# Optimization experiments

Hardware: AMD Instinct MI355X
Metric: run time of the kernel (lower is better)

## Reference

```python
import jax, jax.numpy as jnp
import numpy as np

B, T, D, H = 16, 1024, 512, 8
DH = D // H
NEG = jnp.float32(-2**32 + 1)


def setup_inputs() -> dict:
    key = jax.random.key(0)
    ks = jax.random.split(key, 9)
    s = 1.0 / np.sqrt(D)
    return {
        "queries": jax.random.normal(ks[0], (B, T, D), jnp.float32),
        "keys": jax.random.normal(ks[1], (B, T, D), jnp.float32),
        "value": jax.random.normal(ks[2], (B, T, D), jnp.float32),
        "Wq": jax.random.normal(ks[3], (D, D), jnp.float32) * s,
        "bq": jnp.zeros((D,), jnp.float32),
        "Wk": jax.random.normal(ks[4], (D, D), jnp.float32) * s,
        "bk": jnp.zeros((D,), jnp.float32),
        "Wv": jax.random.normal(ks[5], (D, D), jnp.float32) * s,
        "bv": jnp.zeros((D,), jnp.float32),
    }


def reference(queries, keys, value, Wq, bq, Wk, bk, Wv, bv):
    b, tq, d = queries.shape
    tk = keys.shape[1]
    # linear projections
    Q = queries @ Wq + bq   # [B,Tq,D]
    K = keys @ Wk + bk      # [B,Tk,D]
    V = value @ Wv + bv     # [B,Tk,D]
    # split heads: chunk along feature dim == reshape to [B,T,H,DH]
    Qh = Q.reshape(b, tq, H, DH)
    Kh = K.reshape(b, tk, H, DH)
    Vh = V.reshape(b, tk, H, DH)
    scores = jnp.einsum("bqhd,bkhd->bhqk", Qh, Kh) / jnp.sqrt(jnp.float32(DH))
    # key padding mask: rows of keys summing to 0 are padding
    key_mask = jnp.sign(jnp.abs(keys.sum(axis=-1)))      # [B,Tk]
    scores = jnp.where(key_mask[:, None, None, :] == 0, NEG, scores)
    # causal mask
    causal = jnp.tril(jnp.ones((tq, tk), jnp.float32))   # [Tq,Tk]
    scores = jnp.where(causal[None, None, :, :] == 0, NEG, scores)
    probs = jax.nn.softmax(scores, axis=-1)              # [B,H,Tq,Tk]
    # query padding mask (applied AFTER softmax, as in source)
    query_mask = jnp.sign(jnp.abs(queries.sum(axis=-1)))  # [B,Tq]
    probs = probs * query_mask[:, None, :, None]
    # dropout_rate=0.0 -> identity
    out = jnp.einsum("bhqk,bkhd->bqhd", probs, Vh).reshape(b, tq, d)
    return out + queries  # residual
```

## Files before the change

### kernel.cpp

```cpp
#include <hip/hip_runtime.h>
#include <hip/hip_bf16.h>

#define B_ 16
#define T_ 1024
#define D_ 512
#define H_ 8
#define M_ (B_ * T_)

typedef __attribute__((ext_vector_type(4))) float f32x4;
typedef __attribute__((ext_vector_type(8))) short bf16x8;
typedef __attribute__((ext_vector_type(4))) short bf16x4;

__device__ __forceinline__ void gld_lds16(const void* g, void* l) {
    __builtin_amdgcn_global_load_lds((const __attribute__((address_space(1))) void*)g,
                                     (__attribute__((address_space(3))) void*)l, 16, 0, 0);
}

__device__ __forceinline__ short f2bf(float f) {
    union { float f; unsigned u; } v; v.f = f;
    unsigned r = v.u + 0x7FFF + ((v.u >> 16) & 1);
    return (short)(r >> 16);
}

__global__ void prep_kernel(const float* __restrict__ q, const float* __restrict__ k,
                            const float* __restrict__ v,
                            const float* __restrict__ Wq, const float* __restrict__ Wk,
                            const float* __restrict__ Wv,
                            short* __restrict__ Xbf, short* __restrict__ WtAll,
                            float* __restrict__ qm, float* __restrict__ kb) {
    __shared__ float tile[64][65];
    const int t = threadIdx.x;
    const int mat = blockIdx.y;
    if (blockIdx.x < 64) {
        const float* W = (mat == 0) ? Wq : (mat == 1) ? Wk : Wv;
        short* Wt = WtAll + (size_t)mat * D_ * D_;
        const int kt = ((int)blockIdx.x >> 3) * 64;
        const int nt = ((int)blockIdx.x & 7) * 64;
#pragma unroll
        for (int i = 0; i < 4; ++i) {
            int idx = t + i * 256;
            int r = idx >> 4, c4 = idx & 15;
            float4 vv = *(const float4*)&W[(kt + r) * D_ + nt + c4 * 4];
            tile[r][c4 * 4 + 0] = vv.x; tile[r][c4 * 4 + 1] = vv.y;
            tile[r][c4 * 4 + 2] = vv.z; tile[r][c4 * 4 + 3] = vv.w;
        }
        __syncthreads();
#pragma unroll
        for (int i = 0; i < 2; ++i) {
            int idx = t + i * 256;
            int nr = idx >> 3, c8 = idx & 7;
            bf16x8 pk;
#pragma unroll
            for (int j = 0; j < 8; ++j) pk[j] = f2bf(tile[c8 * 8 + j][nr]);
            *(bf16x8*)&Wt[(nt + nr) * D_ + kt + c8 * 8] = pk;
        }
    } else {
        const int w = t >> 6, lane = t & 63;
        const int row = ((int)blockIdx.x - 64) * 4 + w;
        const float* X = (mat == 0) ? q : (mat == 1) ? k : v;
        short* O = Xbf + (size_t)mat * M_ * D_;
        const float4* p = (const float4*)&X[(size_t)row * D_];
        float4 v0 = p[lane], v1 = p[lane + 64];
        float s = v0.x + v0.y + v0.z + v0.w + v1.x + v1.y + v1.z + v1.w;
#pragma unroll
        for (int m = 1; m < 64; m <<= 1) s += __shfl_xor(s, m);
        bf16x4 p0, p1;
        p0[0] = f2bf(v0.x); p0[1] = f2bf(v0.y); p0[2] = f2bf(v0.z); p0[3] = f2bf(v0.w);
        p1[0] = f2bf(v1.x); p1[1] = f2bf(v1.y); p1[2] = f2bf(v1.z); p1[3] = f2bf(v1.w);
        *(bf16x4*)&O[(size_t)row * D_ + lane * 4] = p0;
        *(bf16x4*)&O[(size_t)row * D_ + 256 + lane * 4] = p1;
        if (lane == 0) {
            if (mat == 0) qm[row] = (s != 0.0f) ? 1.0f : 0.0f;
            else if (mat == 1) kb[row] = (s != 0.0f) ? 0.0f : -3e30f;
        }
    }
}

__global__ __launch_bounds__(256) void proj_gemm_bf(
    const short* __restrict__ Xbf, const short* __restrict__ WtAll,
    const float* __restrict__ bq, const float* __restrict__ bk, const float* __restrict__ bv,
    short* __restrict__ QKV, short* __restrict__ VtG) {
    __shared__ char As[16384];
    __shared__ char Bs[16384];
    const int t = threadIdx.x;
    const int u = blockIdx.x;
    const int wgid = (u & 7) * 192 + (u >> 3);
    const int mat = wgid >> 9;
    const int r = wgid & 511;
    const int m0 = (r >> 2) << 7, n0 = (r & 3) << 7;
    const short* X  = Xbf + (size_t)mat * M_ * D_;
    const short* Wt = WtAll + (size_t)mat * D_ * D_;
    const float* bias = (mat == 0) ? bq : (mat == 1) ? bk : bv;
    short* dst = QKV + (size_t)mat * M_ * D_;
    const int lane = t & 63, w = t >> 6;
    const int wr = w >> 1, wc = w & 1;
    const int cl = lane & 15, g = lane >> 4;

    const int r0 = t >> 3, c0 = ((t & 7) ^ (r0 & 7)) * 8;
    const short* sA = X  + (size_t)(m0 + r0) * D_ + c0;
    const short* sB = Wt + (size_t)(n0 + r0) * D_ + c0;

    f32x4 acc[4][4] = {};
#pragma unroll
    for (int i = 0; i < 4; ++i) {
        gld_lds16(sA + (size_t)(32 * i) * D_, As + t * 16 + i * 4096);
        gld_lds16(sB + (size_t)(32 * i) * D_, Bs + t * 16 + i * 4096);
    }
    for (int kt = 0; kt < D_; kt += 64) {
        __syncthreads();
#pragma unroll
        for (int ks = 0; ks < 2; ++ks) {
            bf16x8 a[4], b[4];
#pragma unroll
            for (int m = 0; m < 4; ++m)
                a[m] = *(const bf16x8*)(As + (wr * 64 + m * 16 + cl) * 128 + (((ks * 4 + g) ^ (cl & 7)) << 4));
#pragma unroll
            for (int n = 0; n < 4; ++n)
                b[n] = *(const bf16x8*)(Bs + (wc * 64 + n * 16 + cl) * 128 + (((ks * 4 + g) ^ (cl & 7)) << 4));
#pragma unroll
            for (int m = 0; m < 4; ++m)
#pragma unroll
                for (int n = 0; n < 4; ++n)
                    acc[m][n] = __builtin_amdgcn_mfma_f32_16x16x32_bf16(a[m], b[n], acc[m][n], 0, 0, 0);
        }
        __syncthreads();
        if (kt + 64 < D_) {
            const int k2 = kt + 64;
#pragma unroll
            for (int i = 0; i < 4; ++i) {
                gld_lds16(sA + (size_t)(32 * i) * D_ + k2, As + t * 16 + i * 4096);
                gld_lds16(sB + (size_t)(32 * i) * D_ + k2, Bs + t * 16 + i * 4096);
            }
        }
    }
    if (VtG != nullptr && mat == 2) {
        const int bb = m0 >> 10, tl0 = m0 & 1023;
#pragma unroll
        for (int n = 0; n < 4; ++n) {
            const int col = n0 + wc * 64 + n * 16 + cl;
            const int h = col >> 6, dh = col & 63;
            short* vrow = VtG + ((size_t)(bb * 8 + h) * 64 + dh) * T_;
            const float bv2 = bias[col];
#pragma unroll
            for (int m = 0; m < 4; ++m) {
                const int tl = tl0 + wr * 64 + m * 16 + g * 4;
                bf16x4 pk;
#pragma unroll
                for (int j = 0; j < 4; ++j) pk[j] = f2bf(acc[m][n][j] + bv2);
                *(bf16x4*)&vrow[tl] = pk;
            }
        }
    } else {
#pragma unroll
        for (int n = 0; n < 4; ++n) {
            int col = n0 + wc * 64 + n * 16 + cl;
            float bv2 = bias[col];
#pragma unroll
            for (int m = 0; m < 4; ++m) {
                int rowb = m0 + wr * 64 + m * 16 + g * 4;
#pragma unroll
                for (int j = 0; j < 4; ++j)
                    dst[(size_t)(rowb + j) * D_ + col] = f2bf(acc[m][n][j] + bv2);
            }
        }
    }
}

__global__ __launch_bounds__(256) void proj_gemm(
    const float* __restrict__ Xq, const float* __restrict__ Xk, const float* __restrict__ Xv,
    const short* __restrict__ WtAll,
    const float* __restrict__ bq, const float* __restrict__ bk, const float* __restrict__ bv,
    short* __restrict__ Qb, short* __restrict__ Kb, short* __restrict__ Vb) {
    __shared__ short As2[128][72];
    __shared__ short Bs2[128][72];
    const int t = threadIdx.x;
    const int mat = blockIdx.z;
    const float* X = (mat == 0) ? Xq : (mat == 1) ? Xk : Xv;
    const short* Wt = WtAll + (size_t)mat * D_ * D_;
    const float* bias = (mat == 0) ? bq : (mat == 1) ? bk : bv;
    short* dst = (mat == 0) ? Qb : (mat == 1) ? Kb : Vb;
    const int m0 = blockIdx.x * 128, n0 = blockIdx.y * 128;
    const int lane = t & 63, w = t >> 6;
    const int wr = w >> 1, wc = w & 1;
    const int cl = lane & 15, g = lane >> 4;
    f32x4 acc[4][4] = {};
    for (int kt = 0; kt < D_; kt += 64) {
#pragma unroll
        for (int i = 0; i < 8; ++i) {
            int idx = t + 256 * i;
            int r = idx >> 4, c4 = idx & 15;
            float4 v = *(const float4*)&X[(size_t)(m0 + r) * D_ + kt + c4 * 4];
            bf16x4 pk;
            pk[0] = f2bf(v.x); pk[1] = f2bf(v.y); pk[2] = f2bf(v.z); pk[3] = f2bf(v.w);
            *(bf16x4*)&As2[r][c4 * 4] = pk;
        }
#pragma unroll
        for (int i = 0; i < 4; ++i) {
            int idx = t + 256 * i;
            int r = idx >> 3, c8 = idx & 7;
            *(bf16x8*)&Bs2[r][c8 * 8] = *(const bf16x8*)&Wt[(size_t)(n0 + r) * D_ + kt + c8 * 8];
        }
        __syncthreads();
#pragma unroll
        for (int ks = 0; ks < 2; ++ks) {
            bf16x8 a[4], b[4];
#pragma unroll
            for (int m = 0; m < 4; ++m)
                a[m] = *(const bf16x8*)&As2[wr * 64 + m * 16 + cl][ks * 32 + g * 8];
#pragma unroll
            for (int n = 0; n < 4; ++n)
                b[n] = *(const bf16x8*)&Bs2[wc * 64 + n * 16 + cl][ks * 32 + g * 8];
#pragma unroll
            for (int m = 0; m < 4; ++m)
#pragma unroll
                for (int n = 0; n < 4; ++n)
                    acc[m][n] = __builtin_amdgcn_mfma_f32_16x16x32_bf16(a[m], b[n], acc[m][n], 0, 0, 0);
        }
        __syncthreads();
    }
#pragma unroll
    for (int n = 0; n < 4; ++n) {
        int col = n0 + wc * 64 + n * 16 + cl;
        float bv2 = bias[col];
#pragma unroll
        for (int m = 0; m < 4; ++m) {
            int rowb = m0 + wr * 64 + m * 16 + g * 4;
#pragma unroll
            for (int j = 0; j < 4; ++j)
                dst[(size_t)(rowb + j) * D_ + col] = f2bf(acc[m][n][j] + bv2);
        }
    }
}

__global__ void mask_kernel(const float* __restrict__ queries, const float* __restrict__ keys,
                            float* __restrict__ qm, float* __restrict__ kb) {
    const int w = threadIdx.x >> 6, lane = threadIdx.x & 63;
    const int row = blockIdx.x * 4 + w;
    const int which = blockIdx.y;
    const float* X = which ? keys : queries;
    const float4* p = (const float4*)&X[(size_t)row * D_];
    float s = 0.f;
#pragma unroll
    for (int i = 0; i < 2; ++i) {
        float4 v = p[lane + 64 * i];
        s += v.x + v.y + v.z + v.w;
    }
#pragma unroll
    for (int m = 1; m < 64; m <<= 1) s += __shfl_xor(s, m);
    if (lane == 0) {
        if (which) kb[row] = (s != 0.0f) ? 0.0f : -3e30f;
        else       qm[row] = (s != 0.0f) ? 1.0f : 0.0f;
    }
}

__global__ void vtrans_kernel(const short* __restrict__ Vb, short* __restrict__ VtG) {
    __shared__ short tile[64][72];
    const int t = threadIdx.x;
    const int kt = blockIdx.x & 15;
    const int h  = (blockIdx.x >> 4) & 7;
    const int b  = blockIdx.x >> 7;
#pragma unroll
    for (int i = 0; i < 2; ++i) {
        int idx = t + i * 256;
        int r = idx >> 3, c8 = idx & 7;
        *(bf16x8*)&tile[((r & 7) << 3) | (r >> 3)][c8 * 8] =
            *(const bf16x8*)&Vb[(size_t)(b * T_ + kt * 64 + r) * D_ + h * 64 + c8 * 8];
    }
    __syncthreads();
#pragma unroll
    for (int i = 0; i < 2; ++i) {
        int idx = t + i * 256;
        int d = idx >> 3, r8 = idx & 7;
        bf16x8 pk;
#pragma unroll
        for (int j = 0; j < 8; ++j) pk[j] = tile[(j << 3) | r8][d];
        *(bf16x8*)&VtG[(size_t)((b * 8 + h) * 64 + d) * T_ + kt * 64 + r8 * 8] = pk;
    }
}

__device__ __forceinline__ void qk_mfma(f32x4 (&s)[4], const char* Kl,
                                        const bf16x8 (&q)[2], int cl, int g) {
#pragma unroll
    for (int kc = 0; kc < 2; ++kc)
#pragma unroll
        for (int nc = 0; nc < 4; ++nc) {
            bf16x8 a = *(const bf16x8*)(Kl + (nc * 16 + cl) * 128 + (((kc * 4 + g) ^ (cl & 7)) << 4));
            s[nc] = __builtin_amdgcn_mfma_f32_16x16x32_bf16(a, q[kc], s[nc], 0, 0, 0);
        }
}

template <bool CAUSAL>
__device__ __forceinline__ void smax_pv(f32x4 (&s)[4], const f32x4 (&kb4)[4],
                                        f32x4 (&o)[4], float& m, float& l,
                                        int qmk, const char* Vl, int cl, int g) {
    const float csc = 0.125f * 1.44269504088896f;
    float pm = -3e30f;
#pragma unroll
    for (int nc = 0; nc < 4; ++nc)
#pragma unroll
        for (int j = 0; j < 4; ++j) {
            float v = fmaf(s[nc][j], csc, kb4[nc][j]);
            if (CAUSAL && (nc * 16 + g * 4 + j > qmk)) v = -3e30f;
            s[nc][j] = v;
            pm = fmaxf(pm, v);
        }
    pm = fmaxf(pm, __shfl_xor(pm, 16));
    pm = fmaxf(pm, __shfl_xor(pm, 32));
    if (__any(pm > m + 8.f)) {
        float mn = fmaxf(m, pm), cf;
        asm("v_exp_f32 %0, %1" : "=v"(cf) : "v"(m - mn));
        l *= cf;
        m = mn;
#pragma unroll
        for (int j = 0; j < 4; ++j) {
            float cfj = __shfl(cf, g * 4 + j);
#pragma unroll
            for (int dc = 0; dc < 4; ++dc) o[dc][j] *= cfj;
        }
    }
    float ps = 0.f;
#pragma unroll
    for (int nc = 0; nc < 4; ++nc)
#pragma unroll
        for (int j = 0; j < 4; ++j) {
            float p;
            asm("v_exp_f32 %0, %1" : "=v"(p) : "v"(s[nc][j] - m));
            s[nc][j] = p;
            ps += p;
        }
    ps += __shfl_xor(ps, 16);
    ps += __shfl_xor(ps, 32);
    l += ps;

    unsigned wp[4][2];
#pragma unroll
    for (int nc = 0; nc < 4; ++nc) {
        asm("v_cvt_pk_bf16_f32 %0, %1, %2" : "=v"(wp[nc][0]) : "v"(s[nc][0]), "v"(s[nc][1]));
        asm("v_cvt_pk_bf16_f32 %0, %1, %2" : "=v"(wp[nc][1]) : "v"(s[nc][2]), "v"(s[nc][3]));
    }
    const bool bp = (g & 1);
#pragma unroll
    for (int ks = 0; ks < 2; ++ks) {
        unsigned A0 = wp[2 * ks][0], A1 = wp[2 * ks][1];
        unsigned B0 = wp[2 * ks + 1][0], B1 = wp[2 * ks + 1][1];
        unsigned snd0 = bp ? A0 : B0, snd1 = bp ? A1 : B1;
        unsigned rcv0 = __shfl_xor(snd0, 16), rcv1 = __shfl_xor(snd1, 16);
        union { unsigned u[4]; bf16x8 v; } pa;
        pa.u[0] = bp ? rcv0 : A0;
        pa.u[1] = bp ? rcv1 : A1;
        pa.u[2] = bp ? B0 : rcv0;
        pa.u[3] = bp ? B1 : rcv1;
        const int vg = ks * 4 + (g & 1) * 2 + (g >> 1);
#pragma unroll
        for (int dc = 0; dc < 4; ++dc) {
            bf16x8 vv = *(const bf16x8*)(Vl + (dc * 16 + cl) * 128 + ((vg ^ (cl & 7)) << 4));
            o[dc] = __builtin_amdgcn_mfma_f32_16x16x32_bf16(pa.v, vv, o[dc], 0, 0, 0);
        }
    }
}

__global__ __launch_bounds__(256, 4) void attn_kernel(
    const short* __restrict__ Qb, const short* __restrict__ Kb,
    const short* __restrict__ VtG, const float* __restrict__ qmask,
    const float* __restrict__ kbias, const float* __restrict__ queries,
    float* __restrict__ out) {
    __shared__ char KV[2][2][8192];
    __shared__ float kbL[1024];
    const int t = threadIdx.x, lane = t & 63, w = t >> 6;
    const int cl = lane & 15, g = lane >> 4;
    const int u = blockIdx.x;
    const int wgid = (u & 7) * 128 + (u >> 3);
    const int pr = wgid & 7, h = (wgid >> 3) & 7, b = wgid >> 6;

    const int rS0 = t >> 3,  cS0 = ((t & 7) ^ (rS0 & 7)) * 8;
    const int t2 = t + 256;
    const int rS1 = t2 >> 3, cS1 = ((t2 & 7) ^ (rS1 & 7)) * 8;
    const short* kS0 = Kb  + ((size_t)(b * T_) + rS0) * D_ + h * 64 + cS0;
    const short* kS1 = Kb  + ((size_t)(b * T_) + rS1) * D_ + h * 64 + cS1;
    const short* vS0 = VtG + (size_t)((b * 8 + h) * 64 + rS0) * T_ + cS0;
    const short* vS1 = VtG + (size_t)((b * 8 + h) * 64 + rS1) * T_ + cS1;

    gld_lds16(kbias + b * T_ + t * 4, (char*)kbL + t * 16);

    int tb = 0;
#pragma unroll
    for (int pass = 0; pass < 2; ++pass) {
        const int qtile = pass ? pr : 15 - pr;
        const int nt = qtile + 1;
        const int qr = qtile * 64 + w * 16 + cl;

        bf16x8 qb[2];
#pragma unroll
        for (int kc = 0; kc < 2; ++kc)
            qb[kc] = *(const bf16x8*)&Qb[(size_t)(b * T_ + qr) * D_ + h * 64 + kc * 32 + g * 8];

        gld_lds16(kS0, &KV[tb][0][0]    + t * 16);
        gld_lds16(kS1, &KV[tb][0][4096] + t * 16);
        gld_lds16(vS0, &KV[tb][1][0]    + t * 16);
        gld_lds16(vS1, &KV[tb][1][4096] + t * 16);

        f32x4 o[4] = {};
        float m = -3e30f, l = 0.f;

        for (int it = 0; it < nt; ++it) {
            __syncthreads();

            f32x4 kb4[4];
#pragma unroll
            for (int nc = 0; nc < 4; ++nc)
                kb4[nc] = *(const f32x4*)((const char*)kbL + it * 256 + nc * 64 + g * 16);

            if (it + 1 < nt) {
                const int kt2 = (it + 1) * 64;
                char* db = &KV[tb ^ 1][0][0];
                gld_lds16(kS0 + (size_t)kt2 * D_, db + t * 16);
                gld_lds16(kS1 + (size_t)kt2 * D_, db + 4096 + t * 16);
                gld_lds16(vS0 + kt2, db + 8192 + t * 16);
                gld_lds16(vS1 + kt2, db + 8192 + 4096 + t * 16);
            }

            const char* Kl = &KV[tb][0][0];
            const char* Vl = &KV[tb][1][0];

            f32x4 s[4] = {};
            qk_mfma(s, Kl, qb, cl, g);
            if (it == nt - 1) smax_pv<true >(s, kb4, o, m, l, w * 16 + cl, Vl, cl, g);
            else              smax_pv<false>(s, kb4, o, m, l, 0,           Vl, cl, g);
            tb ^= 1;
        }

        float inv = 1.0f / l;
#pragma unroll
        for (int j = 0; j < 4; ++j) {
            float linv = __shfl(inv, g * 4 + j);
            const int q = qtile * 64 + w * 16 + g * 4 + j;
            const float sc2 = linv * qmask[b * T_ + q];
            const size_t base = (size_t)(b * T_ + q) * D_ + h * 64;
#pragma unroll
            for (int dc = 0; dc < 4; ++dc) {
                const size_t idx = base + dc * 16 + cl;
                out[idx] = o[dc][j] * sc2 + queries[idx];
            }
        }
    }
}

extern "C" void kernel_launch(void* const* d_in, const int* in_sizes, int n_in,
                              void* d_out, int out_size, void* d_ws, size_t ws_size,
                              hipStream_t stream) {
    const float* queries = (const float*)d_in[0];
    const float* keys    = (const float*)d_in[1];
    const float* value   = (const float*)d_in[2];
    const float* Wq      = (const float*)d_in[3];
    const float* bq      = (const float*)d_in[4];
    const float* Wk      = (const float*)d_in[5];
    const float* bk      = (const float*)d_in[6];
    const float* Wv      = (const float*)d_in[7];
    const float* bv      = (const float*)d_in[8];
    float* out = (float*)d_out;

    char* ws = (char*)d_ws;
    const size_t WT_SZ  = (size_t)D_ * D_ * 2;
    const size_t XB_SZ  = (size_t)M_ * D_ * 2;
    const size_t MASKS  = 2 * (size_t)M_ * 4;

    const size_t NEED_FULL = 3 * WT_SZ + 7 * XB_SZ + MASKS;
    const size_t NEED_MID  = 3 * WT_SZ + 6 * XB_SZ + MASKS;

    if (ws_size >= NEED_FULL) {
        short* WtAll = (short*)(ws);
        short* Xbf   = (short*)(ws + 3 * WT_SZ);
        short* QKV   = (short*)(ws + 3 * WT_SZ + 3 * XB_SZ);
        short* Qb = QKV, *Kb = QKV + M_ * D_;
        short* VtG   = (short*)(ws + 3 * WT_SZ + 6 * XB_SZ);
        float* qm    = (float*)(ws + 3 * WT_SZ + 7 * XB_SZ);
        float* kb    = qm + M_;

        prep_kernel<<<dim3(64 + M_ / 4, 3), 256, 0, stream>>>(
            queries, keys, value, Wq, Wk, Wv, Xbf, WtAll, qm, kb);
        proj_gemm_bf<<<1536, 256, 0, stream>>>(Xbf, WtAll, bq, bk, bv, QKV, VtG);
        attn_kernel<<<1024, 256, 0, stream>>>(Qb, Kb, VtG, qm, kb, queries, out);
    } else if (ws_size >= NEED_MID) {
        short* WtAll = (short*)(ws);
        short* Xbf   = (short*)(ws + 3 * WT_SZ);
        short* QKV   = (short*)(ws + 3 * WT_SZ + 3 * XB_SZ);
        short* Qb = QKV, *Kb = QKV + M_ * D_, *Vb = QKV + 2 * (size_t)M_ * D_;
        short* VtG   = Xbf;
        float* qm    = (float*)(ws + 3 * WT_SZ + 6 * XB_SZ);
        float* kb    = qm + M_;

        prep_kernel<<<dim3(64 + M_ / 4, 3), 256, 0, stream>>>(
            queries, keys, value, Wq, Wk, Wv, Xbf, WtAll, qm, kb);
        proj_gemm_bf<<<1536, 256, 0, stream>>>(Xbf, WtAll, bq, bk, bv, QKV, nullptr);
        vtrans_kernel<<<B_ * H_ * (T_ / 64), 256, 0, stream>>>(Vb, VtG);
        attn_kernel<<<1024, 256, 0, stream>>>(Qb, Kb, VtG, qm, kb, queries, out);
    } else {
        short* WtAll = (short*)(ws);
        short* Qb  = (short*)(ws + 3 * WT_SZ);
        short* Kb  = (short*)(ws + 3 * WT_SZ + XB_SZ);
        short* Vb  = (short*)(ws + 3 * WT_SZ + 2 * XB_SZ);
        short* VtG = (short*)(ws + 3 * WT_SZ + 3 * XB_SZ);
        float* qm  = (float*)(ws + 3 * WT_SZ + 4 * XB_SZ);
        float* kb  = qm + M_;

        prep_kernel<<<dim3(64, 3), 256, 0, stream>>>(
            queries, keys, value, Wq, Wk, Wv, nullptr, WtAll, qm, kb);
        mask_kernel<<<dim3(M_ / 4, 2), 256, 0, stream>>>(queries, keys, qm, kb);
        proj_gemm<<<dim3(M_ / 128, D_ / 128, 3), 256, 0, stream>>>(
            queries, keys, value, WtAll, bq, bk, bv, Qb, Kb, Vb);
        vtrans_kernel<<<B_ * H_ * (T_ / 64), 256, 0, stream>>>(Vb, VtG);
        attn_kernel<<<1024, 256, 0, stream>>>(Qb, Kb, VtG, qm, kb, queries, out);
    }
}
```

Measured before the change: 102.7 us.

## Fuse the two causal query-tile passes to share K/V tile loads

Replaces the two sequential passes over the high and low query tiles with a single loop over key tiles. While the key index is within the low tile's causal range, both query tiles are processed against the same K/V tile already in LDS, which removes the second round of K/V streaming and one pipeline prologue. The cross-lane row-sum reduction of the softmax denominator moves out of the inner loop to the end. In exchange, each thread holds twice the accumulator and score registers in the fused section, which raises spill risk under the existing launch bounds.

```diff
diff --git a/kernel.cpp b/kernel.cpp
--- a/kernel.cpp
+++ b/kernel.cpp
@@ -278,8 +278,8 @@
     }
 }
 
-__device__ __forceinline__ void qk_mfma(f32x4 (&s)[4], const char* Kl,
-                                        const bf16x8 (&q)[2], int cl, int g) {
+__device__ __forceinline__ void qk1(f32x4 (&s)[4], const char* Kl,
+                                    const bf16x8 (&q)[2], int cl, int g) {
 #pragma unroll
     for (int kc = 0; kc < 2; ++kc)
 #pragma unroll
@@ -289,21 +289,36 @@
         }
 }
 
+__device__ __forceinline__ void qk2(f32x4 (&s)[2][4], const char* Kl,
+                                    const bf16x8 (&q)[2][2], int cl, int g) {
+#pragma unroll
+    for (int kc = 0; kc < 2; ++kc)
+#pragma unroll
+        for (int nc = 0; nc < 4; ++nc) {
+            bf16x8 a = *(const bf16x8*)(Kl + (nc * 16 + cl) * 128 + (((kc * 4 + g) ^ (cl & 7)) << 4));
+            s[0][nc] = __builtin_amdgcn_mfma_f32_16x16x32_bf16(a, q[0][kc], s[0][nc], 0, 0, 0);
+            s[1][nc] = __builtin_amdgcn_mfma_f32_16x16x32_bf16(a, q[1][kc], s[1][nc], 0, 0, 0);
+        }
+}
+
+#define CSC_ (0.125f * 1.44269504088896f)
+
 template <bool CAUSAL>
-__device__ __forceinline__ void smax_pv(f32x4 (&s)[4], const f32x4 (&kb4)[4],
-                                        f32x4 (&o)[4], float& m, float& l,
-                                        int qmk, const char* Vl, int cl, int g) {
-    const float csc = 0.125f * 1.44269504088896f;
-    float pm = -3e30f;
-#pragma unroll
-    for (int nc = 0; nc < 4; ++nc)
+__device__ __forceinline__ void smax1(f32x4 (&s)[4], const f32x4 (&kb4)[4],
+                                      f32x4 (&o)[4], float& m, float& l,
+                                      int qmk, const char* Vl, int cl, int g) {
+    float pmn[4];
+#pragma unroll
+    for (int nc = 0; nc < 4; ++nc) {
 #pragma unroll
         for (int j = 0; j < 4; ++j) {
-            float v = fmaf(s[nc][j], csc, kb4[nc][j]);
+            float v = fmaf(s[nc][j], CSC_, kb4[nc][j]);
             if (CAUSAL && (nc * 16 + g * 4 + j > qmk)) v = -3e30f;
             s[nc][j] = v;
-            pm = fmaxf(pm, v);
-        }
+        }
+        pmn[nc] = fmaxf(fmaxf(s[nc][0], s[nc][1]), fmaxf(s[nc][2], s[nc][3]));
+    }
+    float pm = fmaxf(fmaxf(pmn[0], pmn[1]), fmaxf(pmn[2], pmn[3]));
     pm = fmaxf(pm, __shfl_xor(pm, 16));
     pm = fmaxf(pm, __shfl_xor(pm, 32));
     if (__any(pm > m + 8.f)) {
@@ -328,8 +343,6 @@
             s[nc][j] = p;
             ps += p;
         }
-    ps += __shfl_xor(ps, 16);
-    ps += __shfl_xor(ps, 32);
     l += ps;
 
     unsigned wp[4][2];
@@ -355,6 +368,87 @@
         for (int dc = 0; dc < 4; ++dc) {
             bf16x8 vv = *(const bf16x8*)(Vl + (dc * 16 + cl) * 128 + ((vg ^ (cl & 7)) << 4));
             o[dc] = __builtin_amdgcn_mfma_f32_16x16x32_bf16(pa.v, vv, o[dc], 0, 0, 0);
+        }
+    }
+}
+
+template <bool CLO>
+__device__ __forceinline__ void smax2(f32x4 (&s)[2][4], const f32x4 (&kb4)[4],
+                                      f32x4 (&o)[2][4], float (&m)[2], float (&l)[2],
+                                      int qmkLo, const char* Vl, int cl, int g) {
+    float pm[2];
+#pragma unroll
+    for (int tl = 0; tl < 2; ++tl) {
+        float pmn[4];
+#pragma unroll
+        for (int nc = 0; nc < 4; ++nc) {
+#pragma unroll
+            for (int j = 0; j < 4; ++j) {
+                float v = fmaf(s[tl][nc][j], CSC_, kb4[nc][j]);
+                if (tl == 1 && CLO && (nc * 16 + g * 4 + j > qmkLo)) v = -3e30f;
+                s[tl][nc][j] = v;
+            }
+            pmn[nc] = fmaxf(fmaxf(s[tl][nc][0], s[tl][nc][1]), fmaxf(s[tl][nc][2], s[tl][nc][3]));
+        }
+        float p = fmaxf(fmaxf(pmn[0], pmn[1]), fmaxf(pmn[2], pmn[3]));
+        p = fmaxf(p, __shfl_xor(p, 16));
+        p = fmaxf(p, __shfl_xor(p, 32));
+        pm[tl] = p;
+    }
+    if (__any((pm[0] > m[0] + 8.f) || (pm[1] > m[1] + 8.f))) {
+#pragma unroll
+        for (int tl = 0; tl < 2; ++tl) {
+            float mn = fmaxf(m[tl], pm[tl]), cf;
+            asm("v_exp_f32 %0, %1" : "=v"(cf) : "v"(m[tl] - mn));
+            l[tl] *= cf;
+            m[tl] = mn;
+#pragma unroll
+            for (int j = 0; j < 4; ++j) {
+                float cfj = __shfl(cf, g * 4 + j);
+#pragma unroll
+                for (int dc = 0; dc < 4; ++dc) o[tl][dc][j] *= cfj;
+            }
+        }
+    }
+    unsigned wp[2][4][2];
+#pragma unroll
+    for (int tl = 0; tl < 2; ++tl) {
+        float ps = 0.f;
+#pragma unroll
+        for (int nc = 0; nc < 4; ++nc) {
+#pragma unroll
+            for (int j = 0; j < 4; ++j) {
+                float p;
+                asm("v_exp_f32 %0, %1" : "=v"(p) : "v"(s[tl][nc][j] - m[tl]));
+                s[tl][nc][j] = p;
+                ps += p;
+            }
+            asm("v_cvt_pk_bf16_f32 %0, %1, %2" : "=v"(wp[tl][nc][0]) : "v"(s[tl][nc][0]), "v"(s[tl][nc][1]));
+            asm("v_cvt_pk_bf16_f32 %0, %1, %2" : "=v"(wp[tl][nc][1]) : "v"(s[tl][nc][2]), "v"(s[tl][nc][3]));
+        }
+        l[tl] += ps;
+    }
+    const bool bp = (g & 1);
+#pragma unroll
+    for (int ks = 0; ks < 2; ++ks) {
+        union { unsigned u[4]; bf16x8 v; } pa[2];
+#pragma unroll
+        for (int tl = 0; tl < 2; ++tl) {
+            unsigned A0 = wp[tl][2 * ks][0], A1 = wp[tl][2 * ks][1];
+            unsigned B0 = wp[tl][2 * ks + 1][0], B1 = wp[tl][2 * ks + 1][1];
+            unsigned snd0 = bp ? A0 : B0, snd1 = bp ? A1 : B1;
+            unsigned rcv0 = __shfl_xor(snd0, 16), rcv1 = __shfl_xor(snd1, 16);
+            pa[tl].u[0] = bp ? rcv0 : A0;
+            pa[tl].u[1] = bp ? rcv1 : A1;
+            pa[tl].u[2] = bp ? B0 : rcv0;
+            pa[tl].u[3] = bp ? B1 : rcv1;
+        }
+        const int vg = ks * 4 + (g & 1) * 2 + (g >> 1);
+#pragma unroll
+        for (int dc = 0; dc < 4; ++dc) {
+            bf16x8 vv = *(const bf16x8*)(Vl + (dc * 16 + cl) * 128 + ((vg ^ (cl & 7)) << 4));
+            o[0][dc] = __builtin_amdgcn_mfma_f32_16x16x32_bf16(pa[0].v, vv, o[0][dc], 0, 0, 0);
+            o[1][dc] = __builtin_amdgcn_mfma_f32_16x16x32_bf16(pa[1].v, vv, o[1][dc], 0, 0, 0);
         }
     }
 }
@@ -371,6 +465,9 @@
     const int u = blockIdx.x;
     const int wgid = (u & 7) * 128 + (u >> 3);
     const int pr = wgid & 7, h = (wgid >> 3) & 7, b = wgid >> 6;
+    const int ntHi = 16 - pr;
+    const int qrH = (15 - pr) * 64 + w * 16 + cl;
+    const int qrL = pr * 64 + w * 16 + cl;
 
     const int rS0 = t >> 3,  cS0 = ((t & 7) ^ (rS0 & 7)) * 8;
     const int t2 = t + 256;
@@ -382,64 +479,73 @@
 
     gld_lds16(kbias + b * T_ + t * 4, (char*)kbL + t * 16);
 
+    bf16x8 qb[2][2];
+#pragma unroll
+    for (int kc = 0; kc < 2; ++kc) {
+        qb[0][kc] = *(const bf16x8*)&Qb[(size_t)(b * T_ + qrH) * D_ + h * 64 + kc * 32 + g * 8];
+        qb[1][kc] = *(const bf16x8*)&Qb[(size_t)(b * T_ + qrL) * D_ + h * 64 + kc * 32 + g * 8];
+    }
+
+    gld_lds16(kS0, &KV[0][0][0]    + t * 16);
+    gld_lds16(kS1, &KV[0][0][4096] + t * 16);
+    gld_lds16(vS0, &KV[0][1][0]    + t * 16);
+    gld_lds16(vS1, &KV[0][1][4096] + t * 16);
+
+    f32x4 o[2][4] = {};
+    float m[2] = {-3e30f, -3e30f}, l[2] = {0.f, 0.f};
     int tb = 0;
-#pragma unroll
-    for (int pass = 0; pass < 2; ++pass) {
-        const int qtile = pass ? pr : 15 - pr;
-        const int nt = qtile + 1;
-        const int qr = qtile * 64 + w * 16 + cl;
-
-        bf16x8 qb[2];
-#pragma unroll
-        for (int kc = 0; kc < 2; ++kc)
-            qb[kc] = *(const bf16x8*)&Qb[(size_t)(b * T_ + qr) * D_ + h * 64 + kc * 32 + g * 8];
-
-        gld_lds16(kS0, &KV[tb][0][0]    + t * 16);
-        gld_lds16(kS1, &KV[tb][0][4096] + t * 16);
-        gld_lds16(vS0, &KV[tb][1][0]    + t * 16);
-        gld_lds16(vS1, &KV[tb][1][4096] + t * 16);
-
-        f32x4 o[4] = {};
-        float m = -3e30f, l = 0.f;
-
-        for (int it = 0; it < nt; ++it) {
-            __syncthreads();
-
-            f32x4 kb4[4];
-#pragma unroll
-            for (int nc = 0; nc < 4; ++nc)
-                kb4[nc] = *(const f32x4*)((const char*)kbL + it * 256 + nc * 64 + g * 16);
-
-            if (it + 1 < nt) {
-                const int kt2 = (it + 1) * 64;
-                char* db = &KV[tb ^ 1][0][0];
-                gld_lds16(kS0 + (size_t)kt2 * D_, db + t * 16);
-                gld_lds16(kS1 + (size_t)kt2 * D_, db + 4096 + t * 16);
-                gld_lds16(vS0 + kt2, db + 8192 + t * 16);
-                gld_lds16(vS1 + kt2, db + 8192 + 4096 + t * 16);
-            }
-
-            const char* Kl = &KV[tb][0][0];
-            const char* Vl = &KV[tb][1][0];
-
+
+    for (int it = 0; it < ntHi; ++it) {
+        __syncthreads();
+
+        f32x4 kb4[4];
+#pragma unroll
+        for (int nc = 0; nc < 4; ++nc)
+            kb4[nc] = *(const f32x4*)((const char*)kbL + it * 256 + nc * 64 + g * 16);
+
+        if (it + 1 < ntHi) {
+            const int kt2 = (it + 1) * 64;
+            char* db = &KV[tb ^ 1][0][0];
+            gld_lds16(kS0 + (size_t)kt2 * D_, db + t * 16);
+            gld_lds16(kS1 + (size_t)kt2 * D_, db + 4096 + t * 16);
+            gld_lds16(vS0 + kt2, db + 8192 + t * 16);
+            gld_lds16(vS1 + kt2, db + 8192 + 4096 + t * 16);
+        }
+
+        const char* Kl = &KV[tb][0][0];
+        const char* Vl = &KV[tb][1][0];
+
+        if (it <= pr) {
+            f32x4 s2[2][4] = {};
+            qk2(s2, Kl, qb, cl, g);
+            if (it == pr) smax2<true >(s2, kb4, o, m, l, w * 16 + cl, Vl, cl, g);
+            else          smax2<false>(s2, kb4, o, m, l, 0,           Vl, cl, g);
+        } else {
             f32x4 s[4] = {};
-            qk_mfma(s, Kl, qb, cl, g);
-            if (it == nt - 1) smax_pv<true >(s, kb4, o, m, l, w * 16 + cl, Vl, cl, g);
-            else              smax_pv<false>(s, kb4, o, m, l, 0,           Vl, cl, g);
-            tb ^= 1;
-        }
-
-        float inv = 1.0f / l;
+            qk1(s, Kl, qb[0], cl, g);
+            if (it == ntHi - 1) smax1<true >(s, kb4, o[0], m[0], l[0], w * 16 + cl, Vl, cl, g);
+            else                smax1<false>(s, kb4, o[0], m[0], l[0], 0,           Vl, cl, g);
+        }
+        tb ^= 1;
+    }
+
+#pragma unroll
+    for (int tl = 0; tl < 2; ++tl) {
+        float lt = l[tl];
+        lt += __shfl_xor(lt, 16);
+        lt += __shfl_xor(lt, 32);
+        float inv = 1.0f / lt;
+        const int qt = (tl ? pr : 15 - pr) * 64 + w * 16;
 #pragma unroll
         for (int j = 0; j < 4; ++j) {
             float linv = __shfl(inv, g * 4 + j);
-            const int q = qtile * 64 + w * 16 + g * 4 + j;
+            const int q = qt + g * 4 + j;
             const float sc2 = linv * qmask[b * T_ + q];
             const size_t base = (size_t)(b * T_ + q) * D_ + h * 64;
 #pragma unroll
             for (int dc = 0; dc < 4; ++dc) {
                 const size_t idx = base + dc * 16 + cl;
-                out[idx] = o[dc][j] * sc2 + queries[idx];
+                out[idx] = o[tl][dc][j] * sc2 + queries[idx];
             }
         }
     }
```

Measured after the change: 273.5 us. 166% more time.
